# Performance work log

Hardware: AMD Instinct MI355X
Metric: run time of the kernel (lower is better)

## Reference

```python
import jax, jax.numpy as jnp
import numpy as np

N = 50000      # nodes
E = 800000     # edges (avg degree 16)
NFEAT = 256
NHID = 128
NCLASS = 40
NLAYERS_MID = 13  # gc2..gc14


def setup_inputs() -> dict:
    key = jax.random.key(0)
    ks = jax.random.split(key, 16)
    stdv_h = 1.0 / np.sqrt(NHID)     # GraphConvolution stdv = 1/sqrt(out_features)
    stdv_c = 1.0 / np.sqrt(NCLASS)
    u = lambda k, shape, s: jax.random.uniform(k, shape, jnp.float32, -s, s)
    return {
        "x": jax.random.normal(ks[0], (N, NFEAT), jnp.float32),
        "edge_src": jax.random.randint(ks[1], (E,), 0, N, jnp.int32),
        "edge_dst": jax.random.randint(ks[2], (E,), 0, N, jnp.int32),
        "edge_weight": jax.random.uniform(ks[3], (E,), jnp.float32),
        # skip-branch linear (self.weight / self.bias)
        "W0": u(ks[4], (NFEAT, NHID), stdv_h),
        "b0": u(ks[5], (NHID,), stdv_h),
        # gc1: nfeat -> nhid
        "W1": u(ks[6], (NFEAT, NHID), stdv_h),
        "b1": u(ks[7], (NHID,), stdv_h),
        # gc2..gc14: nhid -> nhid, stacked
        "Wmid": u(ks[8], (NLAYERS_MID, NHID, NHID), stdv_h),
        "bmid": u(ks[9], (NLAYERS_MID, NHID), stdv_h),
        # gc15: 14*nhid -> nclass
        "W15": u(ks[10], (14 * NHID, NCLASS), stdv_c),
        "b15": u(ks[11], (NCLASS,), stdv_c),
    }


def reference(x, edge_src, edge_dst, edge_weight, W0, b0, W1, b1, Wmid, bmid, W15, b15):
    n = x.shape[0]

    def gcn(h, W, b):
        # support = h @ W ; out = spmm(adj, support) + b  (adj as weighted edge list)
        support = h @ W
        msgs = support[edge_src] * edge_weight[:, None]           # [E, d]
        agg = jax.ops.segment_sum(msgs, edge_dst, num_segments=n)  # [N, d]
        return agg + b

    z = x @ W0 + b0
    x1 = jax.nn.relu(gcn(x, W1, b1)) + z

    def step(h, Wb):
        W, b = Wb
        hn = jax.nn.relu(gcn(h, W, b)) + h
        return hn, hn

    _, xs = jax.lax.scan(step, x1, (Wmid, bmid))   # xs: [13, N, NHID] = x2..x14
    all_x = jnp.concatenate([x1[None], xs], axis=0)  # [14, N, NHID] = x1..x14
    # concat order in torch code: (x14, x13, ..., x1)
    x_cat = jnp.swapaxes(all_x[::-1], 0, 1).reshape(n, 14 * NHID)
    # dropout is identity in eval mode
    x15 = gcn(x_cat, W15, b15)
    return jax.nn.log_softmax(x15, axis=1)
```

## Files before the change

kernel.cpp:

```cpp
#include <hip/hip_runtime.h>
#include <stdint.h>

#define NN 50000
#define EE 800000
#define DH 128
#define NC 40
#define KCAT (14*DH)
#define CAP 64
#define LP 72

typedef __bf16 bf16x8 __attribute__((ext_vector_type(8)));
typedef float floatx4 __attribute__((ext_vector_type(4)));

__device__ __forceinline__ float bf2f(unsigned short u) {
  union { uint32_t i; float f; } v; v.i = ((uint32_t)u) << 16; return v.f;
}
__device__ __forceinline__ unsigned short f2bf(float f) {
  union { float f; uint32_t i; } v; v.f = f;
  uint32_t x = v.i;
  uint32_t r = (x + 0x7fffu + ((x >> 16) & 1u)) >> 16;
  return (unsigned short)r;
}

__global__ void zero_i32(int* p, int n) {
  int i = blockIdx.x * blockDim.x + threadIdx.x;
  if (i < n) p[i] = 0;
}

__global__ void detect_dtype(const unsigned short* xw, int* wildcnt) {
  int t = threadIdx.x;
  int wild = 0;
  for (int i = t; i < 4096; i += 256) {
    unsigned e = (xw[i] >> 7) & 0xFF;
    if (e >= 0x90) wild++;
  }
  if (wild) atomicAdd(wildcnt, wild);
}

__global__ void convert_f(const void* in, unsigned short* outp, int n, const int* flag) {
  bool isf32 = (*flag) > 32;
  for (int i = blockIdx.x * blockDim.x + threadIdx.x; i < n;
       i += gridDim.x * blockDim.x) {
    outp[i] = isf32 ? f2bf(((const float*)in)[i]) : ((const unsigned short*)in)[i];
  }
}

__global__ void transpose_w(const void* B, unsigned short* BT,
                            int L, int K, int M, int Mpad, const int* flag) {
  bool isf32 = (*flag) > 32;
  int total = L * Mpad * K;
  for (int idx = blockIdx.x * blockDim.x + threadIdx.x; idx < total;
       idx += gridDim.x * blockDim.x) {
    int k = idx % K;
    int n = (idx / K) % Mpad;
    int l = idx / (K * Mpad);
    unsigned short v = 0;
    if (n < M) {
      size_t si = (size_t)l * K * M + (size_t)k * M + n;
      v = isf32 ? f2bf(((const float*)B)[si]) : ((const unsigned short*)B)[si];
    }
    BT[idx] = v;
  }
}

__global__ void build_ell(const int* __restrict__ src, const int* __restrict__ dst,
                          const void* __restrict__ w,
                          int* __restrict__ cnt, int2* __restrict__ ell,
                          const int* __restrict__ flag) {
  bool isf32 = (*flag) > 32;
  int e = blockIdx.x * blockDim.x + threadIdx.x;
  if (e >= EE) return;
  int d = dst[e];
  if ((unsigned)d >= NN) return;
  int p = atomicAdd(&cnt[d], 1);
  if (p >= CAP) return;
  int s = src[e];
  float wf = isf32 ? ((const float*)w)[e] : bf2f(((const unsigned short*)w)[e]);
  if ((unsigned)s >= NN) { s = 0; wf = 0.f; }
  union { float f; int i; } wv; wv.f = wf;
  ell[(size_t)d * CAP + p] = make_int2(s, wv.i);
}

__global__ __launch_bounds__(256) void gemm_h(
    const unsigned short* __restrict__ A, int lda,
    const unsigned short* __restrict__ BT, int K,
    unsigned short* __restrict__ C, const unsigned short* __restrict__ bias) {
  __shared__ unsigned short As[64][LP];
  __shared__ unsigned short Bs[128][LP];
  int t = threadIdx.x;
  int wave = t >> 6, lane = t & 63;
  int q = lane >> 4, mn = lane & 15;
  int r0 = blockIdx.x * 64;
  floatx4 acc[4][2];
  floatx4 zf = {0.f, 0.f, 0.f, 0.f};
  #pragma unroll
  for (int i = 0; i < 4; ++i)
    #pragma unroll
    for (int j = 0; j < 2; ++j) acc[i][j] = zf;

  int arow = t >> 2;
  int akc = (t & 3) << 3;

  for (int k0 = 0; k0 < K; k0 += 32) {
    {
      uint4 v = make_uint4(0, 0, 0, 0);
      if (r0 + arow < NN) v = *(const uint4*)(A + (size_t)(r0 + arow) * lda + k0 + akc);
      *(uint4*)(&As[arow][akc]) = v;
    }
    #pragma unroll
    for (int h = 0; h < 2; ++h) {
      int n = arow + h * 64;
      uint4 v = *(const uint4*)(BT + (size_t)n * K + k0 + akc);
      *(uint4*)(&Bs[n][akc]) = v;
    }
    __syncthreads();
    bf16x8 fa[4], fb[2];
    #pragma unroll
    for (int i = 0; i < 4; ++i) fa[i] = *(const bf16x8*)(&As[i * 16 + mn][q * 8]);
    #pragma unroll
    for (int j = 0; j < 2; ++j) fb[j] = *(const bf16x8*)(&Bs[wave * 32 + j * 16 + mn][q * 8]);
    #pragma unroll
    for (int i = 0; i < 4; ++i)
      #pragma unroll
      for (int j = 0; j < 2; ++j)
        acc[i][j] = __builtin_amdgcn_mfma_f32_16x16x32_bf16(fa[i], fb[j], acc[i][j], 0, 0, 0);
    __syncthreads();
  }
  #pragma unroll
  for (int i = 0; i < 4; ++i) {
    int rbase = r0 + i * 16 + q * 4;
    #pragma unroll
    for (int j = 0; j < 2; ++j) {
      int col = wave * 32 + j * 16 + mn;
      float badd = bias ? bf2f(bias[col]) : 0.0f;
      #pragma unroll
      for (int rr = 0; rr < 4; ++rr) {
        int row = rbase + rr;
        if (row < NN) C[(size_t)row * 128 + col] = f2bf(acc[i][j][rr] + badd);
      }
    }
  }
}

__global__ __launch_bounds__(256) void gemm_cat(
    const unsigned short* __restrict__ A, const unsigned short* __restrict__ BT ,
    float* __restrict__ C) {
  __shared__ unsigned short As[128][LP];
  __shared__ unsigned short Bs[48][LP];
  int t = threadIdx.x;
  int wave = t >> 6, lane = t & 63;
  int q = lane >> 4, mn = lane & 15;
  int r0 = blockIdx.x * 128;
  int kbeg = blockIdx.y * (KCAT / 4), kend = kbeg + KCAT / 4;
  floatx4 acc[2][3];
  floatx4 zf = {0.f, 0.f, 0.f, 0.f};
  #pragma unroll
  for (int i = 0; i < 2; ++i)
    #pragma unroll
    for (int j = 0; j < 3; ++j) acc[i][j] = zf;

  int arow = t >> 2;
  int akc = (t & 3) << 3;

  for (int k0 = kbeg; k0 < kend; k0 += 32) {
    #pragma unroll
    for (int h = 0; h < 2; ++h) {
      int r = arow + h * 64;
      uint4 v = make_uint4(0, 0, 0, 0);
      if (r0 + r < NN) v = *(const uint4*)(A + (size_t)(r0 + r) * KCAT + k0 + akc);
      *(uint4*)(&As[r][akc]) = v;
    }
    if (t < 192) {
      uint4 v = *(const uint4*)(BT + (size_t)arow * KCAT + k0 + akc);
      *(uint4*)(&Bs[arow][akc]) = v;
    }
    __syncthreads();
    bf16x8 fa[2], fb[3];
    #pragma unroll
    for (int i = 0; i < 2; ++i) fa[i] = *(const bf16x8*)(&As[wave * 32 + i * 16 + mn][q * 8]);
    #pragma unroll
    for (int j = 0; j < 3; ++j) fb[j] = *(const bf16x8*)(&Bs[j * 16 + mn][q * 8]);
    #pragma unroll
    for (int i = 0; i < 2; ++i)
      #pragma unroll
      for (int j = 0; j < 3; ++j)
        acc[i][j] = __builtin_amdgcn_mfma_f32_16x16x32_bf16(fa[i], fb[j], acc[i][j], 0, 0, 0);
    __syncthreads();
  }
  #pragma unroll
  for (int i = 0; i < 2; ++i) {
    int rbase = r0 + wave * 32 + i * 16 + q * 4;
    #pragma unroll
    for (int j = 0; j < 3; ++j) {
      int col = j * 16 + mn;
      #pragma unroll
      for (int rr = 0; rr < 4; ++rr) {
        int row = rbase + rr;
        if (row < NN && col < NC)
          atomicAdd(&C[(size_t)row * NC + col], acc[i][j][rr]);
      }
    }
  }
}

__global__ __launch_bounds__(256) void spmm_layer(
    const unsigned short* __restrict__ support, const int* __restrict__ cnt,
    const int2* __restrict__ ell, const unsigned short* __restrict__ bias,
    const unsigned short* __restrict__ res, int res_stride,
    unsigned short* __restrict__ out, int out_stride) {
  int wave = threadIdx.x >> 6, lane = threadIdx.x & 63;
  int row = blockIdx.x * 4 + wave;
  if (row >= NN) return;
  int n = cnt[row];
  if (n > CAP) n = CAP;
  int2 ev = make_int2(0, 0);
  if (lane < n) ev = ell[(size_t)row * CAP + lane];
  float a0 = 0.f, a1 = 0.f;
  int j = 0;
  for (; j + 8 <= n; j += 8) {
    uint32_t g[8];
    int sidx[8];
    #pragma unroll
    for (int u = 0; u < 8; ++u) sidx[u] = __shfl(ev.x, j + u);
    #pragma unroll
    for (int u = 0; u < 8; ++u)
      g[u] = *(const uint32_t*)(support + (size_t)sidx[u] * DH + 2 * lane);
    #pragma unroll
    for (int u = 0; u < 8; ++u) {
      union { int i; float f; } wv; wv.i = __shfl(ev.y, j + u);
      a0 += wv.f * bf2f((unsigned short)(g[u] & 0xffff));
      a1 += wv.f * bf2f((unsigned short)(g[u] >> 16));
    }
  }
  for (; j < n; ++j) {
    int s = __shfl(ev.x, j);
    union { int i; float f; } wv; wv.i = __shfl(ev.y, j);
    uint32_t g = *(const uint32_t*)(support + (size_t)s * DH + 2 * lane);
    a0 += wv.f * bf2f((unsigned short)(g & 0xffff));
    a1 += wv.f * bf2f((unsigned short)(g >> 16));
  }
  uint32_t bw = *(const uint32_t*)(bias + 2 * lane);
  uint32_t rw = *(const uint32_t*)(res + (size_t)row * res_stride + 2 * lane);
  float v0 = fmaxf(a0 + bf2f((unsigned short)(bw & 0xffff)), 0.f) +
             bf2f((unsigned short)(rw & 0xffff));
  float v1 = fmaxf(a1 + bf2f((unsigned short)(bw >> 16)), 0.f) +
             bf2f((unsigned short)(rw >> 16));
  uint32_t o = (uint32_t)f2bf(v0) | ((uint32_t)f2bf(v1) << 16);
  *(uint32_t*)(out + (size_t)row * out_stride + 2 * lane) = o;
}

__global__ __launch_bounds__(256) void spmm_softmax_out(
    const float* __restrict__ s15, const int* __restrict__ cnt,
    const int2* __restrict__ ell, const unsigned short* __restrict__ bias,
    float* __restrict__ out) {
  int wave = threadIdx.x >> 6, lane = threadIdx.x & 63;
  int row = blockIdx.x * 4 + wave;
  if (row >= NN) return;
  int n = cnt[row];
  if (n > CAP) n = CAP;
  int2 ev = make_int2(0, 0);
  if (lane < n) ev = ell[(size_t)row * CAP + lane];
  int fl = lane < NC ? lane : NC - 1;
  float acc = 0.f;
  int j = 0;
  for (; j + 4 <= n; j += 4) {
    float g[4];
    #pragma unroll
    for (int u = 0; u < 4; ++u) {
      int s = __shfl(ev.x, j + u);
      g[u] = s15[(size_t)s * NC + fl];
    }
    #pragma unroll
    for (int u = 0; u < 4; ++u) {
      union { int i; float f; } wv; wv.i = __shfl(ev.y, j + u);
      acc += wv.f * g[u];
    }
  }
  for (; j < n; ++j) {
    int s = __shfl(ev.x, j);
    union { int i; float f; } wv; wv.i = __shfl(ev.y, j);
    acc += wv.f * s15[(size_t)s * NC + fl];
  }
  acc += bf2f(bias[fl]);
  float v = (lane < NC) ? acc : -3.0e38f;
  float m = v;
  #pragma unroll
  for (int off = 32; off > 0; off >>= 1) m = fmaxf(m, __shfl_xor(m, off));
  float e = (lane < NC) ? expf(v - m) : 0.f;
  float sum = e;
  #pragma unroll
  for (int off = 32; off > 0; off >>= 1) sum += __shfl_xor(sum, off);
  if (lane < NC) out[(size_t)row * NC + lane] = v - m - logf(sum);
}

extern "C" void kernel_launch(void* const* d_in, const int* in_sizes, int n_in,
                              void* d_out, int out_size, void* d_ws, size_t ws_size,
                              hipStream_t stream) {
  const void* x   = d_in[0];
  const int* esrc = (const int*)d_in[1];
  const int* edst = (const int*)d_in[2];
  const void* ew  = d_in[3];
  const void* W0  = d_in[4];
  const void* b0  = d_in[5];
  const void* W1  = d_in[6];
  const void* b1  = d_in[7];
  const void* Wm  = d_in[8];
  const void* bm  = d_in[9];
  const void* W15 = d_in[10];
  const void* b15 = d_in[11];
  float* out = (float*)d_out;

  char* ws = (char*)d_ws;
  size_t off = 0;
  auto alloc = [&](size_t bytes) -> void* {
    void* p = ws + off;
    off = (off + bytes + 255) & ~(size_t)255;
    return p;
  };
  unsigned short* xcat = (unsigned short*)alloc((size_t)NN * KCAT * 2);
  unsigned short* xbf  = (unsigned short*)alloc((size_t)NN * 256 * 2);
  unsigned short* supp = (unsigned short*)alloc((size_t)NN * DH * 2);
  unsigned short* zbuf = (unsigned short*)alloc((size_t)NN * DH * 2);
  float* s15           = (float*)alloc((size_t)NN * NC * 4);
  int* counts          = (int*)alloc((size_t)(NN + 1) * 4);
  int2* ell            = (int2*)alloc((size_t)NN * CAP * 8);
  unsigned short* W0T  = (unsigned short*)alloc((size_t)256 * 128 * 2);
  unsigned short* W1T  = (unsigned short*)alloc((size_t)256 * 128 * 2);
  unsigned short* WmT  = (unsigned short*)alloc((size_t)13 * 128 * 128 * 2);
  unsigned short* W15T = (unsigned short*)alloc((size_t)48 * 1792 * 2);
  unsigned short* bb   = (unsigned short*)alloc((size_t)(128 + 128 + 13 * 128 + 40) * 2);
  if (off > ws_size) return;
  int* flag = counts + NN;
  unsigned short* b0b  = bb;
  unsigned short* b1b  = bb + 128;
  unsigned short* bmb  = bb + 256;
  unsigned short* b15b = bb + 256 + 13 * 128;

  zero_i32<<<197, 256, 0, stream>>>(counts, NN + 1);
  zero_i32<<<7813, 256, 0, stream>>>((int*)s15, NN * NC);
  detect_dtype<<<1, 256, 0, stream>>>((const unsigned short*)x, flag);
  transpose_w<<<128, 256, 0, stream>>>(W0, W0T, 1, 256, 128, 128, flag);
  transpose_w<<<128, 256, 0, stream>>>(W1, W1T, 1, 256, 128, 128, flag);
  transpose_w<<<832, 256, 0, stream>>>(Wm, WmT, 13, 128, 128, 128, flag);
  transpose_w<<<336, 256, 0, stream>>>(W15, W15T, 1, 1792, 40, 48, flag);
  convert_f<<<2048, 256, 0, stream>>>(x, xbf, NN * 256, flag);
  convert_f<<<1, 128, 0, stream>>>(b0, b0b, 128, flag);
  convert_f<<<1, 128, 0, stream>>>(b1, b1b, 128, flag);
  convert_f<<<7, 256, 0, stream>>>(bm, bmb, 13 * 128, flag);
  convert_f<<<1, 64, 0, stream>>>(b15, b15b, 40, flag);
  build_ell<<<3125, 256, 0, stream>>>(esrc, edst, ew, counts, ell, flag);

  int gb = (NN + 63) / 64;
  int sb = (NN + 3) / 4;
  gemm_h<<<gb, 256, 0, stream>>>(xbf, 256, W0T, 256, zbuf, b0b);
  gemm_h<<<gb, 256, 0, stream>>>(xbf, 256, W1T, 256, supp, nullptr);
  spmm_layer<<<sb, 256, 0, stream>>>(supp, counts, ell, b1b, zbuf, DH,
                                     xcat + 13 * DH, KCAT);
  for (int l = 0; l < 13; ++l) {
    gemm_h<<<gb, 256, 0, stream>>>(xcat + (13 - l) * DH, KCAT, WmT + l * 128 * 128, 128,
                                   supp, nullptr);
    spmm_layer<<<sb, 256, 0, stream>>>(supp, counts, ell, bmb + l * DH,
                                       xcat + (13 - l) * DH, KCAT,
                                       xcat + (12 - l) * DH, KCAT);
  }
  gemm_cat<<<dim3(391, 4), 256, 0, stream>>>(xcat, W15T, s15);
  spmm_softmax_out<<<sb, 256, 0, stream>>>(s15, counts, ell, b15b, out);
}
```

Baseline: 970.1 us.

## Store layer outputs contiguously and accumulate final projection per layer

Each layer's output now goes to its own contiguous N×128 buffer instead of a strided slice of one wide concatenated matrix. The final 1792→40 GEMM is split into 14 per-layer GEMMs that add into s15 after each layer, with plain adds in place of atomics. gemm_h now stages 128-wide K tiles in LDS and writes its output through LDS as coalesced 16-byte stores. This adds 13 kernel launches and a read-modify-write of the 8 MB fp32 s15 buffer per layer. In exchange it removes the strided concat accesses and the atomic contention of the old split-K GEMM.

```diff
diff --git a/kernel.cpp b/kernel.cpp
--- a/kernel.cpp
+++ b/kernel.cpp
@@ -7,7 +7,7 @@
 #define NC 40
 #define KCAT (14*DH)
 #define CAP 64
-#define LP 72
+#define LPA 136
 
 typedef __bf16 bf16x8 __attribute__((ext_vector_type(8)));
 typedef float floatx4 __attribute__((ext_vector_type(4)));
@@ -83,10 +83,10 @@
 
 __global__ __launch_bounds__(256) void gemm_h(
     const unsigned short* __restrict__ A, int lda,
-    const unsigned short* __restrict__ BT, int K,
+    const unsigned short* __restrict__ BT, int ldb, int K,
     unsigned short* __restrict__ C, const unsigned short* __restrict__ bias) {
-  __shared__ unsigned short As[64][LP];
-  __shared__ unsigned short Bs[128][LP];
+  __shared__ unsigned short As[64][LPA];
+  __shared__ unsigned short Bs[128][LPA];
   int t = threadIdx.x;
   int wave = t >> 6, lane = t & 63;
   int q = lane >> 4, mn = lane & 15;
@@ -99,59 +99,76 @@
     for (int j = 0; j < 2; ++j) acc[i][j] = zf;
 
   int arow = t >> 2;
-  int akc = (t & 3) << 3;
-
-  for (int k0 = 0; k0 < K; k0 += 32) {
+  int akc = (t & 3) << 5;
+  int brow = t >> 1;
+  int bkc = (t & 1) << 6;
+
+  for (int k0 = 0; k0 < K; k0 += 128) {
     {
-      uint4 v = make_uint4(0, 0, 0, 0);
-      if (r0 + arow < NN) v = *(const uint4*)(A + (size_t)(r0 + arow) * lda + k0 + akc);
-      *(uint4*)(&As[arow][akc]) = v;
-    }
-    #pragma unroll
-    for (int h = 0; h < 2; ++h) {
-      int n = arow + h * 64;
-      uint4 v = *(const uint4*)(BT + (size_t)n * K + k0 + akc);
-      *(uint4*)(&Bs[n][akc]) = v;
+      uint4 v[4] = {};
+      if (r0 + arow < NN) {
+        const unsigned short* src = A + (size_t)(r0 + arow) * lda + k0 + akc;
+        #pragma unroll
+        for (int i = 0; i < 4; ++i) v[i] = *(const uint4*)(src + i * 8);
+      }
+      #pragma unroll
+      for (int i = 0; i < 4; ++i) *(uint4*)(&As[arow][akc + i * 8]) = v[i];
+    }
+    {
+      const unsigned short* src = BT + (size_t)brow * ldb + k0 + bkc;
+      #pragma unroll
+      for (int i = 0; i < 8; ++i) {
+        uint4 v = *(const uint4*)(src + i * 8);
+        *(uint4*)(&Bs[brow][bkc + i * 8]) = v;
+      }
     }
     __syncthreads();
-    bf16x8 fa[4], fb[2];
-    #pragma unroll
-    for (int i = 0; i < 4; ++i) fa[i] = *(const bf16x8*)(&As[i * 16 + mn][q * 8]);
-    #pragma unroll
-    for (int j = 0; j < 2; ++j) fb[j] = *(const bf16x8*)(&Bs[wave * 32 + j * 16 + mn][q * 8]);
-    #pragma unroll
-    for (int i = 0; i < 4; ++i)
+    #pragma unroll
+    for (int ks = 0; ks < 4; ++ks) {
+      bf16x8 fa[4], fb[2];
+      #pragma unroll
+      for (int i = 0; i < 4; ++i)
+        fa[i] = *(const bf16x8*)(&As[i * 16 + mn][ks * 32 + q * 8]);
       #pragma unroll
       for (int j = 0; j < 2; ++j)
-        acc[i][j] = __builtin_amdgcn_mfma_f32_16x16x32_bf16(fa[i], fb[j], acc[i][j], 0, 0, 0);
+        fb[j] = *(const bf16x8*)(&Bs[wave * 32 + j * 16 + mn][ks * 32 + q * 8]);
+      #pragma unroll
+      for (int i = 0; i < 4; ++i)
+        #pragma unroll
+        for (int j = 0; j < 2; ++j)
+          acc[i][j] = __builtin_amdgcn_mfma_f32_16x16x32_bf16(fa[i], fb[j], acc[i][j], 0, 0, 0);
+    }
     __syncthreads();
   }
   #pragma unroll
   for (int i = 0; i < 4; ++i) {
-    int rbase = r0 + i * 16 + q * 4;
     #pragma unroll
     for (int j = 0; j < 2; ++j) {
       int col = wave * 32 + j * 16 + mn;
       float badd = bias ? bf2f(bias[col]) : 0.0f;
       #pragma unroll
-      for (int rr = 0; rr < 4; ++rr) {
-        int row = rbase + rr;
-        if (row < NN) C[(size_t)row * 128 + col] = f2bf(acc[i][j][rr] + badd);
-      }
-    }
-  }
-}
-
-__global__ __launch_bounds__(256) void gemm_cat(
-    const unsigned short* __restrict__ A, const unsigned short* __restrict__ BT ,
+      for (int rr = 0; rr < 4; ++rr)
+        As[i * 16 + q * 4 + rr][col] = f2bf(acc[i][j][rr] + badd);
+    }
+  }
+  __syncthreads();
+  if (r0 + arow < NN) {
+    unsigned short* dst = C + (size_t)(r0 + arow) * 128 + ((t & 3) << 5);
+    #pragma unroll
+    for (int i = 0; i < 4; ++i)
+      *(uint4*)(dst + i * 8) = *(const uint4*)(&As[arow][((t & 3) << 5) + i * 8]);
+  }
+}
+
+__global__ __launch_bounds__(256) void gemm_acc(
+    const unsigned short* __restrict__ A, const unsigned short* __restrict__ BT, int ldb,
     float* __restrict__ C) {
-  __shared__ unsigned short As[128][LP];
-  __shared__ unsigned short Bs[48][LP];
+  __shared__ unsigned short As[128][LPA];
+  __shared__ unsigned short Bs[48][LPA];
   int t = threadIdx.x;
   int wave = t >> 6, lane = t & 63;
   int q = lane >> 4, mn = lane & 15;
   int r0 = blockIdx.x * 128;
-  int kbeg = blockIdx.y * (KCAT / 4), kend = kbeg + KCAT / 4;
   floatx4 acc[2][3];
   floatx4 zf = {0.f, 0.f, 0.f, 0.f};
   #pragma unroll
@@ -159,33 +176,43 @@
     #pragma unroll
     for (int j = 0; j < 3; ++j) acc[i][j] = zf;
 
-  int arow = t >> 2;
-  int akc = (t & 3) << 3;
-
-  for (int k0 = kbeg; k0 < kend; k0 += 32) {
-    #pragma unroll
-    for (int h = 0; h < 2; ++h) {
-      int r = arow + h * 64;
-      uint4 v = make_uint4(0, 0, 0, 0);
-      if (r0 + r < NN) v = *(const uint4*)(A + (size_t)(r0 + r) * KCAT + k0 + akc);
-      *(uint4*)(&As[r][akc]) = v;
-    }
-    if (t < 192) {
-      uint4 v = *(const uint4*)(BT + (size_t)arow * KCAT + k0 + akc);
-      *(uint4*)(&Bs[arow][akc]) = v;
-    }
-    __syncthreads();
+  {
+    int arow = t >> 1;
+    int akc = (t & 1) << 6;
+    uint4 v[8] = {};
+    if (r0 + arow < NN) {
+      const unsigned short* src = A + (size_t)(r0 + arow) * 128 + akc;
+      #pragma unroll
+      for (int i = 0; i < 8; ++i) v[i] = *(const uint4*)(src + i * 8);
+    }
+    #pragma unroll
+    for (int i = 0; i < 8; ++i) *(uint4*)(&As[arow][akc + i * 8]) = v[i];
+  }
+  if (t < 192) {
+    int browb = t >> 2;
+    int bkcb = (t & 3) << 5;
+    const unsigned short* src = BT + (size_t)browb * ldb + bkcb;
+    #pragma unroll
+    for (int i = 0; i < 4; ++i) {
+      uint4 v = *(const uint4*)(src + i * 8);
+      *(uint4*)(&Bs[browb][bkcb + i * 8]) = v;
+    }
+  }
+  __syncthreads();
+  #pragma unroll
+  for (int ks = 0; ks < 4; ++ks) {
     bf16x8 fa[2], fb[3];
     #pragma unroll
-    for (int i = 0; i < 2; ++i) fa[i] = *(const bf16x8*)(&As[wave * 32 + i * 16 + mn][q * 8]);
-    #pragma unroll
-    for (int j = 0; j < 3; ++j) fb[j] = *(const bf16x8*)(&Bs[j * 16 + mn][q * 8]);
+    for (int i = 0; i < 2; ++i)
+      fa[i] = *(const bf16x8*)(&As[wave * 32 + i * 16 + mn][ks * 32 + q * 8]);
+    #pragma unroll
+    for (int j = 0; j < 3; ++j)
+      fb[j] = *(const bf16x8*)(&Bs[j * 16 + mn][ks * 32 + q * 8]);
     #pragma unroll
     for (int i = 0; i < 2; ++i)
       #pragma unroll
       for (int j = 0; j < 3; ++j)
         acc[i][j] = __builtin_amdgcn_mfma_f32_16x16x32_bf16(fa[i], fb[j], acc[i][j], 0, 0, 0);
-    __syncthreads();
   }
   #pragma unroll
   for (int i = 0; i < 2; ++i) {
@@ -196,8 +223,7 @@
       #pragma unroll
       for (int rr = 0; rr < 4; ++rr) {
         int row = rbase + rr;
-        if (row < NN && col < NC)
-          atomicAdd(&C[(size_t)row * NC + col], acc[i][j][rr]);
+        if (row < NN && col < NC) C[(size_t)row * NC + col] += acc[i][j][rr];
       }
     }
   }
@@ -206,8 +232,8 @@
 __global__ __launch_bounds__(256) void spmm_layer(
     const unsigned short* __restrict__ support, const int* __restrict__ cnt,
     const int2* __restrict__ ell, const unsigned short* __restrict__ bias,
-    const unsigned short* __restrict__ res, int res_stride,
-    unsigned short* __restrict__ out, int out_stride) {
+    const unsigned short* __restrict__ res,
+    unsigned short* __restrict__ out) {
   int wave = threadIdx.x >> 6, lane = threadIdx.x & 63;
   int row = blockIdx.x * 4 + wave;
   if (row >= NN) return;
@@ -240,13 +266,13 @@
     a1 += wv.f * bf2f((unsigned short)(g >> 16));
   }
   uint32_t bw = *(const uint32_t*)(bias + 2 * lane);
-  uint32_t rw = *(const uint32_t*)(res + (size_t)row * res_stride + 2 * lane);
+  uint32_t rw = *(const uint32_t*)(res + (size_t)row * DH + 2 * lane);
   float v0 = fmaxf(a0 + bf2f((unsigned short)(bw & 0xffff)), 0.f) +
              bf2f((unsigned short)(rw & 0xffff));
   float v1 = fmaxf(a1 + bf2f((unsigned short)(bw >> 16)), 0.f) +
              bf2f((unsigned short)(rw >> 16));
   uint32_t o = (uint32_t)f2bf(v0) | ((uint32_t)f2bf(v1) << 16);
-  *(uint32_t*)(out + (size_t)row * out_stride + 2 * lane) = o;
+  *(uint32_t*)(out + (size_t)row * DH + 2 * lane) = o;
 }
 
 __global__ __launch_bounds__(256) void spmm_softmax_out(
@@ -317,7 +343,7 @@
     off = (off + bytes + 255) & ~(size_t)255;
     return p;
   };
-  unsigned short* xcat = (unsigned short*)alloc((size_t)NN * KCAT * 2);
+  unsigned short* xls  = (unsigned short*)alloc((size_t)14 * NN * DH * 2);
   unsigned short* xbf  = (unsigned short*)alloc((size_t)NN * 256 * 2);
   unsigned short* supp = (unsigned short*)alloc((size_t)NN * DH * 2);
   unsigned short* zbuf = (unsigned short*)alloc((size_t)NN * DH * 2);
@@ -335,6 +361,7 @@
   unsigned short* b1b  = bb + 128;
   unsigned short* bmb  = bb + 256;
   unsigned short* b15b = bb + 256 + 13 * 128;
+  auto xl = [&](int l) { return xls + (size_t)(l - 1) * NN * DH; };
 
   zero_i32<<<197, 256, 0, stream>>>(counts, NN + 1);
   zero_i32<<<7813, 256, 0, stream>>>((int*)s15, NN * NC);
@@ -351,18 +378,18 @@
   build_ell<<<3125, 256, 0, stream>>>(esrc, edst, ew, counts, ell, flag);
 
   int gb = (NN + 63) / 64;
+  int ab = (NN + 127) / 128;
   int sb = (NN + 3) / 4;
-  gemm_h<<<gb, 256, 0, stream>>>(xbf, 256, W0T, 256, zbuf, b0b);
-  gemm_h<<<gb, 256, 0, stream>>>(xbf, 256, W1T, 256, supp, nullptr);
-  spmm_layer<<<sb, 256, 0, stream>>>(supp, counts, ell, b1b, zbuf, DH,
-                                     xcat + 13 * DH, KCAT);
-  for (int l = 0; l < 13; ++l) {
-    gemm_h<<<gb, 256, 0, stream>>>(xcat + (13 - l) * DH, KCAT, WmT + l * 128 * 128, 128,
+  gemm_h<<<gb, 256, 0, stream>>>(xbf, 256, W0T, 256, 256, zbuf, b0b);
+  gemm_h<<<gb, 256, 0, stream>>>(xbf, 256, W1T, 256, 256, supp, nullptr);
+  spmm_layer<<<sb, 256, 0, stream>>>(supp, counts, ell, b1b, zbuf, xl(1));
+  gemm_acc<<<ab, 256, 0, stream>>>(xl(1), W15T + 13 * 128, KCAT, s15);
+  for (int l = 1; l <= 13; ++l) {
+    gemm_h<<<gb, 256, 0, stream>>>(xl(l), 128, WmT + (l - 1) * 128 * 128, 128, 128,
                                    supp, nullptr);
-    spmm_layer<<<sb, 256, 0, stream>>>(supp, counts, ell, bmb + l * DH,
-                                       xcat + (13 - l) * DH, KCAT,
-                                       xcat + (12 - l) * DH, KCAT);
-  }
-  gemm_cat<<<dim3(391, 4), 256, 0, stream>>>(xcat, W15T, s15);
+    spmm_layer<<<sb, 256, 0, stream>>>(supp, counts, ell, bmb + (l - 1) * DH,
+                                       xl(l), xl(l + 1));
+    gemm_acc<<<ab, 256, 0, stream>>>(xl(l + 1), W15T + (13 - l) * 128, KCAT, s15);
+  }
   spmm_softmax_out<<<sb, 256, 0, stream>>>(s15, counts, ell, b15b, out);
 }
```

New measurement: 1.187 ms. 22.3% more time.
